# Performance work log

Hardware: AMD Instinct MI355X
Metric: run time of the kernel (lower is better)

## Reference

```python
import jax, jax.numpy as jnp
import numpy as np

TOPK = 8
EPS = 1e-12  # matches torch F.normalize default eps


def setup_inputs() -> dict:
    key = jax.random.key(0)
    x = jax.random.normal(key, (8, 2048, 128), dtype=jnp.float32)
    return {"x": x}


def reference(x) -> jnp.ndarray:
    B, N, D = x.shape
    # --- pairwise dot scores on L2-normalized features (cosine similarity) ---
    norm = jnp.sqrt(jnp.sum(x * x, axis=-1, keepdims=True))
    normed = x / jnp.maximum(norm, EPS)
    scores = jnp.einsum('bnd,bmd->bnm', normed, normed)  # [B, N, N]

    # --- top-k per row -> binary adjacency via scatter ---
    _, idx = jax.lax.top_k(scores, TOPK)  # [B, N, k]
    bi = jnp.arange(B)[:, None, None]
    ni = jnp.arange(N)[None, :, None]
    adj = jnp.zeros((B, N, N), dtype=x.dtype).at[bi, ni, idx].set(1.0)

    # --- symmetrize and add self loops ---
    adj = jnp.maximum(adj, jnp.swapaxes(adj, 1, 2))
    eye = jnp.eye(N, dtype=x.dtype)
    adj = jnp.maximum(adj, eye[None, :, :])
    return adj
```

## Files before the change

kernel.cpp:

```cpp
#include <hip/hip_runtime.h>
#include <cstdint>

#define NN 2048
#define DD 128
#define BATCH 8
#define NROWS 16384
#define MARGIN 0.02f
#define CAP2 64

typedef __attribute__((ext_vector_type(8))) short bf16x8;
typedef __attribute__((ext_vector_type(4))) float f32x4;
typedef unsigned long long u64;
typedef unsigned int u32;
typedef unsigned short u16;

__device__ __forceinline__ u32 bf16rne(float f) {
  u32 u = __float_as_uint(f);
  return (u + 0x7fffu + ((u >> 16) & 1u)) >> 16;
}
__device__ __forceinline__ u32 bf16up(float f) {
  const u32 u = __float_as_uint(f);
  return (u + (((int)u >= 0) ? 0xFFFFu : 0u)) >> 16;
}

__global__ __launch_bounds__(256) void k_normalize(const float* __restrict__ x,
                                                   double* __restrict__ rinv,
                                                   u32* __restrict__ nb,
                                                   float4* __restrict__ outz) {
  const int wave = threadIdx.x >> 6, lane = threadIdx.x & 63;
  const long long row = (long long)blockIdx.x * 4 + wave;
  float2 v = ((const float2*)(x + row * DD))[lane];
  const double d0 = v.x, d1 = v.y;
  double s = d0 * d0 + d1 * d1;
  #pragma unroll
  for (int m = 32; m >= 1; m >>= 1) s += __shfl_xor(s, m, 64);
  double den = sqrt(s); den = den > 1e-12 ? den : 1e-12;
  if (lane == 0) rinv[row] = 1.0 / den;
  double2 o; o.x = d0 / den; o.y = d1 / den;
  nb[row * (DD / 2) + lane] = bf16rne((float)o.x) | (bf16rne((float)o.y) << 16);

  {
    const int base = blockIdx.x * 256 + threadIdx.x;
    const float4 zf = {0.0f, 0.0f, 0.0f, 0.0f};
    #pragma unroll
    for (int k = 0; k < 8; ++k) outz[base + k * 1048576] = zf;
  }
}

#define CXF(i, j) { const float a_ = L[i], b_ = L[j]; L[i] = fmaxf(a_, b_); L[j] = fminf(a_, b_); }
__device__ __forceinline__ void merge8f(float (&kv)[8], const float (&ov)[8]) {
  float L[8];
  #pragma unroll
  for (int i = 0; i < 8; ++i) L[i] = fmaxf(kv[i], ov[7 - i]);
  CXF(0, 4) CXF(1, 5) CXF(2, 6) CXF(3, 7)
  CXF(0, 2) CXF(1, 3) CXF(4, 6) CXF(5, 7)
  CXF(0, 1) CXF(2, 3) CXF(4, 5) CXF(6, 7)
  #pragma unroll
  for (int i = 0; i < 8; ++i) kv[i] = L[i];
}

__device__ __forceinline__ u64 make_key(double s, int col) {
  u64 u = (u64)__double_as_longlong(s);
  const u64 m = (u64)((long long)u >> 63);
  u ^= (m | 0x8000000000000000ull);
  return (u & ~2047ull) | (u64)(2047 - col);
}
__device__ __forceinline__ u64 umax64(u64 a, u64 b) { return a > b ? a : b; }
__device__ __forceinline__ u64 umin64(u64 a, u64 b) { return a > b ? b : a; }
__device__ __forceinline__ void merge8(u64 (&kv)[8], const u64 (&ov)[8]) {
  u64 L[8];
  #pragma unroll
  for (int i = 0; i < 8; ++i) L[i] = umax64(kv[i], ov[7 - i]);
#define CX(i, j) { const u64 a_ = L[i], b_ = L[j]; L[i] = umax64(a_, b_); L[j] = umin64(a_, b_); }
  CX(0, 4) CX(1, 5) CX(2, 6) CX(3, 7)
  CX(0, 2) CX(1, 3) CX(4, 6) CX(5, 7)
  CX(0, 1) CX(2, 3) CX(4, 5) CX(6, 7)
#undef CX
  #pragma unroll
  for (int i = 0; i < 8; ++i) kv[i] = L[i];
}
__device__ __forceinline__ void insert8u(u64 (&v)[8], u64 nk) {
  if (nk > v[7]) {
    v[7] = nk;
    #pragma unroll
    for (int q = 7; q >= 1; --q) {
      const u64 a = v[q - 1], b = v[q];
      const bool sw = b > a;
      v[q - 1] = sw ? b : a; v[q] = sw ? a : b;
    }
  }
}

__global__ __launch_bounds__(1024, 4) void k_build(const u32* __restrict__ nb,
                                                   u32* __restrict__ gcnt,
                                                   u32* __restrict__ gcand) {
  __shared__ float bmf[32][130];
  __shared__ float thl[32];
  __shared__ u32 cnt[32];
  __shared__ u32 cand[32][CAP2];

  const int tid = threadIdx.x; const int w = tid >> 6; const int l = tid & 63;
  const int q = l >> 4; const int m = l & 15;
  const int b = blockIdx.x & 7;
  const int rowblk = blockIdx.x >> 3;
  const int row0 = b * NN + rowblk * 32;
  const long long brow = (long long)b * NN;

  bf16x8 pvals = {0,0,0,0,0,0,0,0}, pones = {0,0,0,0,0,0,0,0};
  if (q == 0) {
    pvals[0] = (short)(__float_as_uint((float)(m + 1)) >> 16);
    pones[0] = (short)(__float_as_uint(1.0f) >> 16);
  }
  const f32x4 z4 = {0.0f, 0.0f, 0.0f, 0.0f};
  const f32x4 pr  = __builtin_amdgcn_mfma_f32_16x16x32_bf16(pvals, pones, z4, 0, 0, 0);
  const f32x4 pr2 = __builtin_amdgcn_mfma_f32_16x16x32_bf16(pones, pvals, z4, 0, 0, 0);
  int cof[4];
  #pragma unroll
  for (int p = 0; p < 4; ++p) cof[p] = (int)pr[p] - 1;
  const int rof = (int)pr2[0] - 1;

  if (tid < 32) cnt[tid] = 0u;

  bf16x8 ar4[2][4];
  #pragma unroll
  for (int rf = 0; rf < 2; ++rf) {
    const u32* Ap = nb + (long long)(row0 + 16 * rf + m) * (DD / 2) + 4 * q;
    #pragma unroll
    for (int cc = 0; cc < 4; ++cc) ar4[rf][cc] = *(const bf16x8*)(Ap + 16 * cc);
  }

  const int c0w = w * 128;
  const u32* Bb = nb + (brow + c0w) * (DD / 2);
  bf16x8 bcA[4], bcB[4];
  uint2 pk[16];

#define LOADB(DST, T) { const u32* p_ = Bb + (long long)(16 * (T) + m) * (DD / 2) + 4 * q; \
  _Pragma("unroll") for (int cc = 0; cc < 4; ++cc) DST[cc] = *(const bf16x8*)(p_ + 16 * cc); }
#define TILE1(BC, T) {                                                             \
    _Pragma("unroll") for (int rf = 0; rf < 2; ++rf) {                             \
      f32x4 acc = z4;                                                              \
      _Pragma("unroll") for (int cc = 0; cc < 4; ++cc)                             \
        acc = __builtin_amdgcn_mfma_f32_16x16x32_bf16(BC[cc], ar4[rf][cc], acc, 0, 0, 0); \
      float bm_ = fmaxf(fmaxf(acc[0], acc[1]), fmaxf(acc[2], acc[3]));             \
      bm_ = fmaxf(bm_, __shfl_xor(bm_, 16, 64));                                   \
      bm_ = fmaxf(bm_, __shfl_xor(bm_, 32, 64));                                   \
      if (q == 0) bmf[16 * rf + m][w * 8 + (T)] = bm_;                             \
      pk[(T) * 2 + rf].x = bf16up(acc[0]) | (bf16up(acc[1]) << 16);                \
      pk[(T) * 2 + rf].y = bf16up(acc[2]) | (bf16up(acc[3]) << 16);                \
    } }

  LOADB(bcA, 0)
  #pragma unroll
  for (int t = 0; t < 8; t += 2) {
    LOADB(bcB, t + 1)
    TILE1(bcA, t)
    if (t + 2 < 8) LOADB(bcA, t + 2)
    TILE1(bcB, t + 1)
  }
#undef LOADB
#undef TILE1
  __syncthreads();

  for (int j = 0; j < 2; ++j) {
    const int rib = w * 2 + j;
    const float b0 = bmf[rib][2 * l];
    const float b1 = bmf[rib][2 * l + 1];
    float mx = fmaxf(b0, b1);
    float kv8[8];
    {
      const float o  = __shfl_xor(mx, 1, 64);
      const float h2 = fmaxf(mx, o), l2 = fminf(mx, o);
      const float p0 = __shfl_xor(h2, 2, 64), p1 = __shfl_xor(l2, 2, 64);
      const float m0 = fmaxf(h2, p0);
      const float xx = fminf(h2, p0);
      const float yy = fmaxf(l2, p1);
      const float m3 = fminf(l2, p1);
      const float m1 = fmaxf(xx, yy);
      const float m2 = fminf(xx, yy);
      const float q0 = __shfl_xor(m0, 4, 64), q1 = __shfl_xor(m1, 4, 64);
      const float q2 = __shfl_xor(m2, 4, 64), q3 = __shfl_xor(m3, 4, 64);
      float L[8] = {m0, m1, m2, m3, q3, q2, q1, q0};
      CXF(0, 4) CXF(1, 5) CXF(2, 6) CXF(3, 7)
      CXF(0, 2) CXF(1, 3) CXF(4, 6) CXF(5, 7)
      CXF(0, 1) CXF(2, 3) CXF(4, 5) CXF(6, 7)
      #pragma unroll
      for (int s = 0; s < 8; ++s) kv8[s] = L[s];
      #pragma unroll
      for (int mk = 8; mk <= 32; mk <<= 1) {
        float ov[8];
        #pragma unroll
        for (int s = 0; s < 8; ++s) ov[s] = __shfl_xor(kv8[s], mk, 64);
        merge8f(kv8, ov);
      }
    }
    if (l == 0) thl[rib] = kv8[7] - MARGIN;
  }
  __syncthreads();

  {
    float th2[2]; int rib2[2];
    #pragma unroll
    for (int rf = 0; rf < 2; ++rf) {
      rib2[rf] = 16 * rf + rof;
      th2[rf] = thl[rib2[rf]];
    }
    #pragma unroll
    for (int t = 0; t < 8; ++t)
      #pragma unroll
      for (int rf = 0; rf < 2; ++rf) {
        const uint2 pv = pk[t * 2 + rf];
        const float v0 = __uint_as_float(pv.x << 16);
        const float v1 = __uint_as_float(pv.x & 0xFFFF0000u);
        const float v2 = __uint_as_float(pv.y << 16);
        const float v3 = __uint_as_float(pv.y & 0xFFFF0000u);
        #pragma unroll
        for (int p = 0; p < 4; ++p) {
          const float vv = (p == 0) ? v0 : (p == 1) ? v1 : (p == 2) ? v2 : v3;
          if (vv >= th2[p & 0] + 0.0f * p, vv >= th2[rf]) {
            const u32 id = atomicAdd(&cnt[rib2[rf]], 1u);
            if (id < CAP2) cand[rib2[rf]][id] = (u32)(c0w + 16 * t + cof[p]);
          }
        }
      }
  }
  __syncthreads();

  {
    const int row = tid >> 5;
    const int sl = tid & 31;
    if (sl == 0) gcnt[row0 + row] = cnt[row];
    gcand[(long long)(row0 + row) * CAP2 + sl] = cand[row][sl];
    gcand[(long long)(row0 + row) * CAP2 + sl + 32] = cand[row][sl + 32];
  }
}

__global__ __launch_bounds__(256) void k_rescore(const u32* __restrict__ gcnt,
                                                 const u32* __restrict__ gcand,
                                                 const float* __restrict__ x,
                                                 const double* __restrict__ rinv,
                                                 float* __restrict__ out) {
  const int w = threadIdx.x >> 6, l = threadIdx.x & 63;
  const int q = l >> 4, m = l & 15;
  const int b = blockIdx.x & 7;
  const int idx = blockIdx.x >> 3;
  const int r = b * NN + idx * 4 + w;
  const int n = r & (NN - 1);
  const long long brow = r - n;

  const int c = (int)gcnt[r];
  const double ri = rinv[r];
  u64 kv[8];
  #pragma unroll
  for (int s = 0; s < 8; ++s) kv[s] = 0ull;

  if (c <= CAP2) {
    float2 a4[4];
    #pragma unroll
    for (int jj = 0; jj < 4; ++jj)
      a4[jj] = ((const float2*)(x + (long long)r * DD))[m + 16 * jj];
    const u32* crow = gcand + (long long)r * CAP2;

    for (int i = 0; i < c; i += 4) {
      const int gi = i + q;
      const bool valid = gi < c;
      const int col = valid ? (int)crow[gi] : 0;
      const float2* cp = (const float2*)(x + (brow + col) * DD);
      double d = 0.0;
      #pragma unroll
      for (int jj = 0; jj < 4; ++jj) {
        const float2 bv = cp[m + 16 * jj];
        d = fma((double)a4[jj].x, (double)bv.x, d);
        d = fma((double)a4[jj].y, (double)bv.y, d);
      }
      #pragma unroll
      for (int mk = 1; mk <= 8; mk <<= 1) d += __shfl_xor(d, mk, 64);
      if (valid) insert8u(kv, make_key(d * ri * rinv[brow + col], col));
    }
    #pragma unroll
    for (int mk = 16; mk <= 32; mk <<= 1) {
      u64 ov[8];
      #pragma unroll
      for (int s = 0; s < 8; ++s) ov[s] = __shfl_xor(kv[s], mk, 64);
      merge8(kv, ov);
    }
  } else {
    for (int base = 0; base < NN; base += 64) {
      const int col = base + l;
      const float* ap = x + (long long)r * DD;
      const float* cp2 = x + (brow + col) * DD;
      double d = 0.0;
      for (int kk = 0; kk < 64; ++kk) {
        const float2 av = ((const float2*)ap)[kk];
        const float2 bv = ((const float2*)cp2)[kk];
        d = fma((double)av.x, (double)bv.x, fma((double)av.y, (double)bv.y, d));
      }
      d = d * ri * rinv[brow + col];
      u64 one[8];
      one[0] = make_key(d, col);
      #pragma unroll
      for (int s = 1; s < 8; ++s) one[s] = 0ull;
      #pragma unroll
      for (int mk = 1; mk <= 32; mk <<= 1) {
        u64 ov[8];
        #pragma unroll
        for (int s = 0; s < 8; ++s) ov[s] = __shfl_xor(one[s], mk, 64);
        merge8(one, ov);
      }
      merge8(kv, one);
    }
  }

  const long long orow = (long long)r * NN;
  const long long obase = brow * NN;
  if (l == 8) out[orow + n] = 1.0f;
  #pragma unroll
  for (int s = 0; s < 8; ++s) {
    const int mcol = 2047 - (int)(kv[s] & 2047ull);
    if (l == s) {
      out[orow + mcol] = 1.0f;
      out[obase + (long long)mcol * NN + n] = 1.0f;
    }
  }
}

extern "C" void kernel_launch(void* const* d_in, const int* in_sizes, int n_in,
                              void* d_out, int out_size, void* d_ws, size_t ws_size,
                              hipStream_t stream) {
  const float* x = (const float*)d_in[0];
  float* out = (float*)d_out;
  char* ws = (char*)d_ws;
  u32* nb = (u32*)ws;
  double* rinv = (double*)(ws + 4194304);
  u32* gcnt = (u32*)(ws + 4325376);
  u32* gcand = (u32*)(ws + 4390912);

  hipLaunchKernelGGL(k_normalize, dim3(NROWS / 4), dim3(256), 0, stream, x, rinv, nb,
                     (float4*)out);
  hipLaunchKernelGGL(k_build, dim3(512), dim3(1024), 0, stream, nb, gcnt, gcand);
  hipLaunchKernelGGL(k_rescore, dim3(NROWS / 4), dim3(256), 0, stream, gcnt, gcand,
                     x, rinv, out);
}
```

Baseline: 233.2 us.

## Fuse candidate rescoring into build kernel, dropping global candidate buffers

```diff
diff --git a/kernel.cpp b/kernel.cpp
--- a/kernel.cpp
+++ b/kernel.cpp
@@ -91,9 +91,10 @@
   }
 }
 
-__global__ __launch_bounds__(1024, 4) void k_build(const u32* __restrict__ nb,
-                                                   u32* __restrict__ gcnt,
-                                                   u32* __restrict__ gcand) {
+__global__ __launch_bounds__(1024, 8) void k_build(const u32* __restrict__ nb,
+                                                   const float* __restrict__ x,
+                                                   const double* __restrict__ rinv,
+                                                   float* __restrict__ out) {
   __shared__ float bmf[32][130];
   __shared__ float thl[32];
   __shared__ u32 cnt[32];
@@ -216,7 +217,7 @@
         #pragma unroll
         for (int p = 0; p < 4; ++p) {
           const float vv = (p == 0) ? v0 : (p == 1) ? v1 : (p == 2) ? v2 : v3;
-          if (vv >= th2[p & 0] + 0.0f * p, vv >= th2[rf]) {
+          if (vv >= th2[rf]) {
             const u32 id = atomicAdd(&cnt[rib2[rf]], 1u);
             if (id < CAP2) cand[rib2[rf]][id] = (u32)(c0w + 16 * t + cof[p]);
           }
@@ -225,100 +226,82 @@
   }
   __syncthreads();
 
-  {
-    const int row = tid >> 5;
-    const int sl = tid & 31;
-    if (sl == 0) gcnt[row0 + row] = cnt[row];
-    gcand[(long long)(row0 + row) * CAP2 + sl] = cand[row][sl];
-    gcand[(long long)(row0 + row) * CAP2 + sl + 32] = cand[row][sl + 32];
-  }
-}
-
-__global__ __launch_bounds__(256) void k_rescore(const u32* __restrict__ gcnt,
-                                                 const u32* __restrict__ gcand,
-                                                 const float* __restrict__ x,
-                                                 const double* __restrict__ rinv,
-                                                 float* __restrict__ out) {
-  const int w = threadIdx.x >> 6, l = threadIdx.x & 63;
-  const int q = l >> 4, m = l & 15;
-  const int b = blockIdx.x & 7;
-  const int idx = blockIdx.x >> 3;
-  const int r = b * NN + idx * 4 + w;
-  const int n = r & (NN - 1);
-  const long long brow = r - n;
-
-  const int c = (int)gcnt[r];
-  const double ri = rinv[r];
-  u64 kv[8];
-  #pragma unroll
-  for (int s = 0; s < 8; ++s) kv[s] = 0ull;
-
-  if (c <= CAP2) {
-    float2 a4[4];
-    #pragma unroll
-    for (int jj = 0; jj < 4; ++jj)
-      a4[jj] = ((const float2*)(x + (long long)r * DD))[m + 16 * jj];
-    const u32* crow = gcand + (long long)r * CAP2;
-
-    for (int i = 0; i < c; i += 4) {
-      const int gi = i + q;
-      const bool valid = gi < c;
-      const int col = valid ? (int)crow[gi] : 0;
-      const float2* cp = (const float2*)(x + (brow + col) * DD);
-      double d = 0.0;
-      #pragma unroll
-      for (int jj = 0; jj < 4; ++jj) {
-        const float2 bv = cp[m + 16 * jj];
-        d = fma((double)a4[jj].x, (double)bv.x, d);
-        d = fma((double)a4[jj].y, (double)bv.y, d);
-      }
-      #pragma unroll
-      for (int mk = 1; mk <= 8; mk <<= 1) d += __shfl_xor(d, mk, 64);
-      if (valid) insert8u(kv, make_key(d * ri * rinv[brow + col], col));
-    }
-    #pragma unroll
-    for (int mk = 16; mk <= 32; mk <<= 1) {
-      u64 ov[8];
-      #pragma unroll
-      for (int s = 0; s < 8; ++s) ov[s] = __shfl_xor(kv[s], mk, 64);
-      merge8(kv, ov);
-    }
-  } else {
-    for (int base = 0; base < NN; base += 64) {
-      const int col = base + l;
-      const float* ap = x + (long long)r * DD;
-      const float* cp2 = x + (brow + col) * DD;
-      double d = 0.0;
-      for (int kk = 0; kk < 64; ++kk) {
-        const float2 av = ((const float2*)ap)[kk];
-        const float2 bv = ((const float2*)cp2)[kk];
-        d = fma((double)av.x, (double)bv.x, fma((double)av.y, (double)bv.y, d));
-      }
-      d = d * ri * rinv[brow + col];
-      u64 one[8];
-      one[0] = make_key(d, col);
-      #pragma unroll
-      for (int s = 1; s < 8; ++s) one[s] = 0ull;
-      #pragma unroll
-      for (int mk = 1; mk <= 32; mk <<= 1) {
+  for (int j = 0; j < 2; ++j) {
+    const int rib = w * 2 + j;
+    const int r = row0 + rib;
+    const int n = r & (NN - 1);
+    const int c = (int)cnt[rib];
+    const double ri = rinv[r];
+    u64 kv[8];
+    #pragma unroll
+    for (int s = 0; s < 8; ++s) kv[s] = 0ull;
+
+    if (c <= CAP2) {
+      float2 a4[4];
+      #pragma unroll
+      for (int jj = 0; jj < 4; ++jj)
+        a4[jj] = ((const float2*)(x + (long long)r * DD))[m + 16 * jj];
+
+      for (int i = 0; i < c; i += 4) {
+        const int gi = i + q;
+        const bool valid = gi < c;
+        const int col = valid ? (int)cand[rib][gi] : 0;
+        const float2* cp = (const float2*)(x + (brow + col) * DD);
+        double d = 0.0;
+        #pragma unroll
+        for (int jj = 0; jj < 4; ++jj) {
+          const float2 bv = cp[m + 16 * jj];
+          d = fma((double)a4[jj].x, (double)bv.x, d);
+          d = fma((double)a4[jj].y, (double)bv.y, d);
+        }
+        #pragma unroll
+        for (int mk = 1; mk <= 8; mk <<= 1) d += __shfl_xor(d, mk, 64);
+        if (valid) insert8u(kv, make_key(d * ri * rinv[brow + col], col));
+      }
+      #pragma unroll
+      for (int mk = 16; mk <= 32; mk <<= 1) {
         u64 ov[8];
         #pragma unroll
-        for (int s = 0; s < 8; ++s) ov[s] = __shfl_xor(one[s], mk, 64);
-        merge8(one, ov);
-      }
-      merge8(kv, one);
-    }
-  }
-
-  const long long orow = (long long)r * NN;
-  const long long obase = brow * NN;
-  if (l == 8) out[orow + n] = 1.0f;
-  #pragma unroll
-  for (int s = 0; s < 8; ++s) {
-    const int mcol = 2047 - (int)(kv[s] & 2047ull);
-    if (l == s) {
-      out[orow + mcol] = 1.0f;
-      out[obase + (long long)mcol * NN + n] = 1.0f;
+        for (int s = 0; s < 8; ++s) ov[s] = __shfl_xor(kv[s], mk, 64);
+        merge8(kv, ov);
+      }
+    } else {
+      for (int base = 0; base < NN; base += 64) {
+        const int col = base + l;
+        const float* ap = x + (long long)r * DD;
+        const float* cp2 = x + (brow + col) * DD;
+        double d = 0.0;
+        for (int kk = 0; kk < 64; ++kk) {
+          const float2 av = ((const float2*)ap)[kk];
+          const float2 bv = ((const float2*)cp2)[kk];
+          d = fma((double)av.x, (double)bv.x, fma((double)av.y, (double)bv.y, d));
+        }
+        d = d * ri * rinv[brow + col];
+        u64 one[8];
+        one[0] = make_key(d, col);
+        #pragma unroll
+        for (int s = 1; s < 8; ++s) one[s] = 0ull;
+        #pragma unroll
+        for (int mk = 1; mk <= 32; mk <<= 1) {
+          u64 ov[8];
+          #pragma unroll
+          for (int s = 0; s < 8; ++s) ov[s] = __shfl_xor(one[s], mk, 64);
+          merge8(one, ov);
+        }
+        merge8(kv, one);
+      }
+    }
+
+    const long long orow = (long long)r * NN;
+    const long long obase = brow * NN;
+    if (l == 8) out[orow + n] = 1.0f;
+    #pragma unroll
+    for (int s = 0; s < 8; ++s) {
+      const int mcol = 2047 - (int)(kv[s] & 2047ull);
+      if (l == s) {
+        out[orow + mcol] = 1.0f;
+        out[obase + (long long)mcol * NN + n] = 1.0f;
+      }
     }
   }
 }
@@ -331,12 +314,8 @@
   char* ws = (char*)d_ws;
   u32* nb = (u32*)ws;
   double* rinv = (double*)(ws + 4194304);
-  u32* gcnt = (u32*)(ws + 4325376);
-  u32* gcand = (u32*)(ws + 4390912);
 
   hipLaunchKernelGGL(k_normalize, dim3(NROWS / 4), dim3(256), 0, stream, x, rinv, nb,
                      (float4*)out);
-  hipLaunchKernelGGL(k_build, dim3(512), dim3(1024), 0, stream, nb, gcnt, gcand);
-  hipLaunchKernelGGL(k_rescore, dim3(NROWS / 4), dim3(256), 0, stream, gcnt, gcand,
-                     x, rinv, out);
-}
+  hipLaunchKernelGGL(k_build, dim3(512), dim3(1024), 0, stream, nb, x, rinv, out);
+}
```

New measurement: 329.4 us. +41.2%, slower.
